# Performance work log

Measured on AMD Instinct MI355X. Metric: run time of the kernel, lower is better.

Reference implementation:

```python
import jax, jax.numpy as jnp
import numpy as np

DIM = 1024
NUM_HEADS = 16
HEAD_DIM = DIM // NUM_HEADS
SCALE = HEAD_DIM ** -0.5


def setup_inputs() -> dict:
    key = jax.random.key(0)
    ks = jax.random.split(key, 5)
    x = jax.random.normal(ks[0], (4, 1024, DIM), dtype=jnp.float32)
    w_qkv = jax.random.normal(ks[1], (DIM, 3 * DIM), dtype=jnp.float32) * (DIM ** -0.5)
    b_qkv = jnp.zeros((3 * DIM,), dtype=jnp.float32)
    w_proj = jax.random.normal(ks[2], (DIM, DIM), dtype=jnp.float32) * (DIM ** -0.5)
    b_proj = jnp.zeros((DIM,), dtype=jnp.float32)
    return {"x": x, "w_qkv": w_qkv, "b_qkv": b_qkv, "w_proj": w_proj, "b_proj": b_proj}


def reference(x, w_qkv, b_qkv, w_proj, b_proj):
    B, N, C = x.shape
    qkv = x @ w_qkv + b_qkv                                  # [B, N, 3C]
    qkv = qkv.reshape(B, N, 3, NUM_HEADS, HEAD_DIM)
    qkv = jnp.transpose(qkv, (2, 0, 3, 1, 4))                # [3, B, H, N, d]
    q, k, v = qkv[0] * SCALE, qkv[1], qkv[2]
    # attn scores in float32 (clamp to finfo range is a no-op after the cast)
    attn = jnp.einsum('bhnd,bhmd->bhnm', q, k).astype(jnp.float32)
    f32 = jnp.finfo(jnp.float32)
    attn = jnp.clip(attn, f32.min, f32.max)
    attn = jax.nn.softmax(attn, axis=-1)
    out = jnp.einsum('bhnm,bhmd->bhnd', attn, v)             # [B, H, N, d]
    out = jnp.transpose(out, (0, 2, 1, 3)).reshape(B, N, C)
    return out @ w_proj + b_proj
```

## Files before the change

### kernel.cpp

```cpp
#include <hip/hip_runtime.h>


typedef _Float16 half8 __attribute__((ext_vector_type(8)));
typedef _Float16 half4v __attribute__((ext_vector_type(4)));
typedef float floatx4 __attribute__((ext_vector_type(4)));

#define MFMA16(a, b, c) __builtin_amdgcn_mfma_f32_16x16x32_f16((a), (b), (c), 0, 0, 0)

static constexpr int DIM = 1024;
static constexpr int BATCH = 4;
static constexpr int SEQ = 1024;
static constexpr int NH = 16;
static constexpr int HD = 64;
static constexpr float SCALE = 0.125f;

__device__ static inline void gld16(_Float16* lds, const _Float16* g) {
    __builtin_amdgcn_global_load_lds(
        (const __attribute__((address_space(1))) void*)g,
        (__attribute__((address_space(3))) void*)lds, 16, 0, 0);
}

__global__ __launch_bounds__(256) void prep(const float* __restrict__ x,
                                            _Float16* __restrict__ xh,
                                            const float* __restrict__ wqkv,
                                            _Float16* __restrict__ wqkvT,
                                            const float* __restrict__ wproj,
                                            _Float16* __restrict__ wprojT) {
    __shared__ float tile[32][33];
    const int bid = blockIdx.x;
    const int tid = threadIdx.x;
    if (bid < 4096) {
        int i = (bid * 256 + tid) * 4;
        float4 v = *reinterpret_cast<const float4*>(x + i);
        half4v h;
        h[0] = (_Float16)v.x; h[1] = (_Float16)v.y;
        h[2] = (_Float16)v.z; h[3] = (_Float16)v.w;
        const int m = i >> 10, k = i & 1023;
        *reinterpret_cast<half4v*>(
            &xh[((size_t)(k >> 5) * 4096 + m) * 32 + (k & 31)]) = h;
        return;
    }
    const float* in;
    _Float16* out;
    int C, NN, bx, by;
    if (bid < 7168) {
        int b = bid - 4096;
        in = wqkv; out = wqkvT; C = 3072; NN = 3072;
        bx = b % 96; by = b / 96;
    } else {
        int b = bid - 7168;
        in = wproj; out = wprojT; C = 1024; NN = 1024;
        bx = b & 31; by = b >> 5;
    }
    const int c0 = bx * 32, r0 = by * 32;
    const int tx = tid & 31, ty = tid >> 5;
#pragma unroll
    for (int j = 0; j < 32; j += 8)
        tile[ty + j][tx] = in[(size_t)(r0 + ty + j) * C + (c0 + tx)];
    __syncthreads();
#pragma unroll
    for (int j = 0; j < 32; j += 8)
        out[((size_t)(r0 >> 5) * NN + (c0 + ty + j)) * 32 + tx] =
            (_Float16)tile[tx][ty + j];
}

template <int MODE>
__global__ __launch_bounds__(256, 2) void gemm_bt(const _Float16* __restrict__ A,
                                                  const _Float16* __restrict__ Bt,
                                                  const float* __restrict__ bias, int N,
                                                  float* __restrict__ outF,
                                                  _Float16* __restrict__ qbuf,
                                                  _Float16* __restrict__ kbuf,
                                                  _Float16* __restrict__ vtbuf) {
    constexpr int NT = 32;
    __shared__ _Float16 Ah[3 * 4096];
    __shared__ _Float16 Bh[3 * 4096];

    const int tid = threadIdx.x;
    const int wid = tid >> 6;
    const int lane = tid & 63;
    const int g = lane >> 4;
    const int ln = lane & 15;
    const int wr = wid >> 1, wc = wid & 1;
    const int m0 = blockIdx.y * 128;
    const int n0 = blockIdx.x * 128;
    const size_t PA = (size_t)4096 * 32;
    const size_t PB = (size_t)N * 32;
    const int woff = wid * 1024;
    const int lsw = (lane >> 2) * 32 + (((lane & 3) ^ ((lane >> 3) & 3)) * 8);
    const int gsw = (g ^ ((ln >> 1) & 3)) * 8;
    const _Float16* ga = A + (size_t)m0 * 32 + woff + lsw;
    const _Float16* gb = Bt + (size_t)n0 * 32 + woff + lsw;

    floatx4 acc[4][4];
#pragma unroll
    for (int i = 0; i < 4; ++i)
#pragma unroll
        for (int j = 0; j < 4; ++j) acc[i][j] = (floatx4){0.f, 0.f, 0.f, 0.f};

#pragma unroll
    for (int t = 0; t < 2; ++t) {
        gld16(&Ah[t * 4096 + woff], ga + t * PA);
        gld16(&Ah[t * 4096 + woff + 512], ga + t * PA + 512);
        gld16(&Bh[t * 4096 + woff], gb + t * PB);
        gld16(&Bh[t * 4096 + woff + 512], gb + t * PB + 512);
    }

    for (int kt = 0; kt < NT; ++kt) {
        if (kt < NT - 1) asm volatile("s_waitcnt vmcnt(4)" ::: "memory");
        else             asm volatile("s_waitcnt vmcnt(0)" ::: "memory");
        asm volatile("s_barrier" ::: "memory");
        if (kt < NT - 2) {
            const int pf = (kt + 2) % 3;
            const size_t ka = (size_t)(kt + 2) * PA;
            const size_t kb = (size_t)(kt + 2) * PB;
            gld16(&Ah[pf * 4096 + woff], ga + ka);
            gld16(&Ah[pf * 4096 + woff + 512], ga + ka + 512);
            gld16(&Bh[pf * 4096 + woff], gb + kb);
            gld16(&Bh[pf * 4096 + woff + 512], gb + kb + 512);
        }
        const _Float16* Ac = &Ah[(kt % 3) * 4096];
        const _Float16* Bc = &Bh[(kt % 3) * 4096];

        half8 af[4], bf[4];
#pragma unroll
        for (int i = 0; i < 4; ++i)
            af[i] = *reinterpret_cast<const half8*>(
                &Ac[(wr * 64 + i * 16 + ln) * 32 + gsw]);
#pragma unroll
        for (int j = 0; j < 4; ++j)
            bf[j] = *reinterpret_cast<const half8*>(
                &Bc[(wc * 64 + j * 16 + ln) * 32 + gsw]);
#pragma unroll
        for (int i = 0; i < 4; ++i)
#pragma unroll
            for (int j = 0; j < 4; ++j) acc[i][j] = MFMA16(af[i], bf[j], acc[i][j]);
    }

#pragma unroll
    for (int i = 0; i < 4; ++i) {
#pragma unroll
        for (int j = 0; j < 4; ++j) {
            const int n = n0 + wc * 64 + j * 16 + ln;
            const float bn = bias[n];
            const int mrow = m0 + wr * 64 + i * 16 + g * 4;
            if (MODE == 0) {
                const int which = n >> 10;
                const int rem = n & 1023;
                const int h = rem >> 6;
                const int dd = rem & 63;
                const int b = mrow >> 10, tok = mrow & 1023;
                const int bh = b * NH + h;
                if (which == 2) {
                    half4v pk;
#pragma unroll
                    for (int r = 0; r < 4; ++r) pk[r] = (_Float16)(acc[i][j][r] + bn);
                    *reinterpret_cast<half4v*>(
                        &vtbuf[((size_t)(bh * 32 + (tok >> 5)) * 64 + dd) * 32 +
                               (tok & 31)]) = pk;
                } else if (which == 1) {
#pragma unroll
                    for (int r = 0; r < 4; ++r)
                        kbuf[((size_t)(bh * 2 + (dd >> 5)) * SEQ + tok + r) * 32 +
                             (dd & 31)] = (_Float16)(acc[i][j][r] + bn);
                } else {
#pragma unroll
                    for (int r = 0; r < 4; ++r)
                        qbuf[(size_t)((bh << 10) + tok + r) * HD + dd] =
                            (_Float16)((acc[i][j][r] + bn) * SCALE);
                }
            } else {
#pragma unroll
                for (int r = 0; r < 4; ++r)
                    outF[(size_t)(mrow + r) * N + n] = acc[i][j][r] + bn;
            }
        }
    }
}

__global__ __launch_bounds__(256, 2) void flash_attn(const _Float16* __restrict__ qbuf,
                                                     const _Float16* __restrict__ kbuf,
                                                     const _Float16* __restrict__ vtbuf,
                                                     _Float16* __restrict__ attn_out) {
    __shared__ _Float16 Klds[3 * 4096];
    __shared__ _Float16 Vlds[3 * 4096];
    __shared__ _Float16 Plds[8 * 16 * 68];

    const int tid = threadIdx.x;
    const int wid = tid >> 6;
    const int lane = tid & 63;
    const int g = lane >> 4;
    const int ln = lane & 15;
    const int bh = blockIdx.x;
    const int qbase = blockIdx.y * 128 + wid * 32;
    const _Float16* qg = qbuf + ((size_t)bh << 10) * HD;
    const _Float16* kg = kbuf + (size_t)bh * (2 * SEQ * 32);
    const _Float16* vg = vtbuf + (size_t)bh * (32 * 64 * 32);

    const int woff = wid * 512;
    const int lsw = (lane >> 2) * 32 + (((lane & 3) ^ ((lane >> 3) & 3)) * 8);
    const int gsw = (g ^ ((ln >> 1) & 3)) * 8;

    half8 qf[2][2];
#pragma unroll
    for (int rg = 0; rg < 2; ++rg)
#pragma unroll
        for (int f = 0; f < 2; ++f)
            qf[rg][f] = *reinterpret_cast<const half8*>(
                qg + (size_t)(qbase + rg * 16 + ln) * HD + f * 32 + g * 8);

    floatx4 o[2][4];
#pragma unroll
    for (int rg = 0; rg < 2; ++rg)
#pragma unroll
        for (int t = 0; t < 4; ++t) o[rg][t] = (floatx4){0.f, 0.f, 0.f, 0.f};
    float l_lane[2][4] = {{0.f, 0.f, 0.f, 0.f}, {0.f, 0.f, 0.f, 0.f}};

    _Float16* Pw = Plds + wid * (2 * 16 * 68);

    constexpr int NT = SEQ / 64;
#pragma unroll
    for (int t = 0; t < 2; ++t) {
#pragma unroll
        for (int f = 0; f < 2; ++f) {
            gld16(&Klds[t * 4096 + f * 2048 + woff],
                  kg + (size_t)f * (SEQ * 32) + t * 64 * 32 + woff + lsw);
            gld16(&Vlds[t * 4096 + f * 2048 + woff],
                  vg + (size_t)(2 * t + f) * 2048 + woff + lsw);
        }
    }

    for (int kt = 0; kt < NT; ++kt) {
        if (kt < NT - 1) asm volatile("s_waitcnt vmcnt(4)" ::: "memory");
        else             asm volatile("s_waitcnt vmcnt(0)" ::: "memory");
        asm volatile("s_barrier" ::: "memory");
        if (kt < NT - 2) {
            const int pf = (kt + 2) % 3;
            const int krp = (kt + 2) * 64;
#pragma unroll
            for (int f = 0; f < 2; ++f) {
                gld16(&Klds[pf * 4096 + f * 2048 + woff],
                      kg + (size_t)f * (SEQ * 32) + krp * 32 + woff + lsw);
                gld16(&Vlds[pf * 4096 + f * 2048 + woff],
                      vg + (size_t)(2 * (kt + 2) + f) * 2048 + woff + lsw);
            }
        }
        const _Float16* Kb = &Klds[(kt % 3) * 4096];
        const _Float16* Vb = &Vlds[(kt % 3) * 4096];

        half8 kf[4][2], vf[4][2];
#pragma unroll
        for (int c = 0; c < 4; ++c)
#pragma unroll
            for (int f = 0; f < 2; ++f) {
                kf[c][f] = *reinterpret_cast<const half8*>(
                    &Kb[f * 2048 + (c * 16 + ln) * 32 + gsw]);
                vf[c][f] = *reinterpret_cast<const half8*>(
                    &Vb[f * 2048 + (c * 16 + ln) * 32 + gsw]);
            }

        floatx4 s[2][4];
#pragma unroll
        for (int rg = 0; rg < 2; ++rg)
#pragma unroll
            for (int c = 0; c < 4; ++c) {
                floatx4 z = (floatx4){0.f, 0.f, 0.f, 0.f};
                z = MFMA16(qf[rg][0], kf[c][0], z);
                z = MFMA16(qf[rg][1], kf[c][1], z);
                s[rg][c] = z;
            }

#pragma unroll
        for (int rg = 0; rg < 2; ++rg)
#pragma unroll
            for (int c = 0; c < 4; ++c)
#pragma unroll
                for (int r = 0; r < 4; ++r) {
                    float p = __expf(s[rg][c][r]);
                    l_lane[rg][r] += p;
                    Pw[(rg * 16 + g * 4 + r) * 68 + c * 16 + ln] = (_Float16)p;
                }

        asm volatile("s_waitcnt lgkmcnt(0)" ::: "memory");

#pragma unroll
        for (int rg = 0; rg < 2; ++rg) {
            half8 pf0 = *reinterpret_cast<const half8*>(&Pw[(rg * 16 + ln) * 68 + g * 8]);
            half8 pf1 = *reinterpret_cast<const half8*>(&Pw[(rg * 16 + ln) * 68 + 32 + g * 8]);
#pragma unroll
            for (int t = 0; t < 4; ++t) {
                o[rg][t] = MFMA16(pf0, vf[t][0], o[rg][t]);
                o[rg][t] = MFMA16(pf1, vf[t][1], o[rg][t]);
            }
        }
    }

    const int b = bh >> 4, h = bh & 15;
#pragma unroll
    for (int rg = 0; rg < 2; ++rg)
#pragma unroll
        for (int r = 0; r < 4; ++r) {
            float l = l_lane[rg][r];
            l += __shfl_xor(l, 1);
            l += __shfl_xor(l, 2);
            l += __shfl_xor(l, 4);
            l += __shfl_xor(l, 8);
            const float inv = 1.0f / l;
            const int tok = qbase + rg * 16 + g * 4 + r;
#pragma unroll
            for (int t = 0; t < 4; ++t)
                attn_out[((size_t)(h * 2 + (t >> 1)) * 4096 + (b * SEQ + tok)) * 32 +
                         (t & 1) * 16 + ln] = (_Float16)(o[rg][t][r] * inv);
        }
}

extern "C" void kernel_launch(void* const* d_in, const int* in_sizes, int n_in,
                              void* d_out, int out_size, void* d_ws, size_t ws_size,
                              hipStream_t stream) {
    const float* x = (const float*)d_in[0];
    const float* wqkv = (const float*)d_in[1];
    const float* bqkv = (const float*)d_in[2];
    const float* wproj = (const float*)d_in[3];
    const float* bproj = (const float*)d_in[4];
    float* out = (float*)d_out;

    char* ws = (char*)d_ws;
    _Float16* xh     = (_Float16*)(ws);
    _Float16* wqkvT  = (_Float16*)(ws + (8ull << 20));
    _Float16* qbuf   = (_Float16*)(ws + (14ull << 20));
    _Float16* kbuf   = (_Float16*)(ws + (22ull << 20));
    _Float16* vtbuf  = (_Float16*)(ws + (30ull << 20));
    _Float16* wprojT = (_Float16*)(ws + (38ull << 20));
    _Float16* attn   = xh;

    prep<<<8192, 256, 0, stream>>>(x, xh, wqkv, wqkvT, wproj, wprojT);
    gemm_bt<0><<<dim3(24, 32), 256, 0, stream>>>(xh, wqkvT, bqkv, 3 * DIM, nullptr,
                                                 qbuf, kbuf, vtbuf);
    flash_attn<<<dim3(BATCH * NH, SEQ / 128), 256, 0, stream>>>(qbuf, kbuf, vtbuf, attn);
    gemm_bt<1><<<dim3(8, 32), 256, 0, stream>>>(attn, wprojT, bproj, DIM, out,
                                                nullptr, nullptr, nullptr);
}
```

Baseline: 181.6 us.

## Compute transposed scores and pass P through lane shuffles instead of LDS

Flash attention now computes S^T = K·Q^T so each wave handles 16 query rows. The fp16-packed probabilities are rearranged into the A-operand layout with cross-lane shuffles, which removes the per-wave P scratch in LDS and its write/read round trip. The K/V pipeline drops from triple to double buffering with a full vmcnt(0) wait each iteration. The grid doubles with launch bounds raised to 4 blocks per CU. This trades less K/V reuse per block and a shallower prefetch for lower LDS use, fewer registers and more occupancy.

Result: faster. 177.2 us (-2.4%).

```diff
diff --git a/kernel.cpp b/kernel.cpp
--- a/kernel.cpp
+++ b/kernel.cpp
@@ -3,6 +3,7 @@
 
 typedef _Float16 half8 __attribute__((ext_vector_type(8)));
 typedef _Float16 half4v __attribute__((ext_vector_type(4)));
+typedef __fp16 fp16x2 __attribute__((ext_vector_type(2)));
 typedef float floatx4 __attribute__((ext_vector_type(4)));
 
 #define MFMA16(a, b, c) __builtin_amdgcn_mfma_f32_16x16x32_f16((a), (b), (c), 0, 0, 0)
@@ -178,13 +179,12 @@
     }
 }
 
-__global__ __launch_bounds__(256, 2) void flash_attn(const _Float16* __restrict__ qbuf,
+__global__ __launch_bounds__(256, 4) void flash_attn(const _Float16* __restrict__ qbuf,
                                                      const _Float16* __restrict__ kbuf,
                                                      const _Float16* __restrict__ vtbuf,
                                                      _Float16* __restrict__ attn_out) {
-    __shared__ _Float16 Klds[3 * 4096];
-    __shared__ _Float16 Vlds[3 * 4096];
-    __shared__ _Float16 Plds[8 * 16 * 68];
+    __shared__ _Float16 Klds[2 * 4096];
+    __shared__ _Float16 Vlds[2 * 4096];
 
     const int tid = threadIdx.x;
     const int wid = tid >> 6;
@@ -192,7 +192,7 @@
     const int g = lane >> 4;
     const int ln = lane & 15;
     const int bh = blockIdx.x;
-    const int qbase = blockIdx.y * 128 + wid * 32;
+    const int qbase = blockIdx.y * 64 + wid * 16;
     const _Float16* qg = qbuf + ((size_t)bh << 10) * HD;
     const _Float16* kg = kbuf + (size_t)bh * (2 * SEQ * 32);
     const _Float16* vg = vtbuf + (size_t)bh * (32 * 64 * 32);
@@ -200,53 +200,43 @@
     const int woff = wid * 512;
     const int lsw = (lane >> 2) * 32 + (((lane & 3) ^ ((lane >> 3) & 3)) * 8);
     const int gsw = (g ^ ((ln >> 1) & 3)) * 8;
-
-    half8 qf[2][2];
-#pragma unroll
-    for (int rg = 0; rg < 2; ++rg)
-#pragma unroll
-        for (int f = 0; f < 2; ++f)
-            qf[rg][f] = *reinterpret_cast<const half8*>(
-                qg + (size_t)(qbase + rg * 16 + ln) * HD + f * 32 + g * 8);
-
-    floatx4 o[2][4];
-#pragma unroll
-    for (int rg = 0; rg < 2; ++rg)
-#pragma unroll
-        for (int t = 0; t < 4; ++t) o[rg][t] = (floatx4){0.f, 0.f, 0.f, 0.f};
-    float l_lane[2][4] = {{0.f, 0.f, 0.f, 0.f}, {0.f, 0.f, 0.f, 0.f}};
-
-    _Float16* Pw = Plds + wid * (2 * 16 * 68);
+    const int sl0 = ((lane >> 4) & 1) * 32 + ln;
+    const bool hi32 = (lane & 32) != 0;
+
+    half8 qf[2];
+#pragma unroll
+    for (int f = 0; f < 2; ++f)
+        qf[f] = *reinterpret_cast<const half8*>(
+            qg + (size_t)(qbase + ln) * HD + f * 32 + g * 8);
+
+    floatx4 o[4];
+#pragma unroll
+    for (int t = 0; t < 4; ++t) o[t] = (floatx4){0.f, 0.f, 0.f, 0.f};
+    float l_lane = 0.f;
 
     constexpr int NT = SEQ / 64;
 #pragma unroll
-    for (int t = 0; t < 2; ++t) {
-#pragma unroll
-        for (int f = 0; f < 2; ++f) {
-            gld16(&Klds[t * 4096 + f * 2048 + woff],
-                  kg + (size_t)f * (SEQ * 32) + t * 64 * 32 + woff + lsw);
-            gld16(&Vlds[t * 4096 + f * 2048 + woff],
-                  vg + (size_t)(2 * t + f) * 2048 + woff + lsw);
-        }
+    for (int f = 0; f < 2; ++f) {
+        gld16(&Klds[f * 2048 + woff], kg + (size_t)f * (SEQ * 32) + woff + lsw);
+        gld16(&Vlds[f * 2048 + woff], vg + (size_t)f * 2048 + woff + lsw);
     }
 
     for (int kt = 0; kt < NT; ++kt) {
-        if (kt < NT - 1) asm volatile("s_waitcnt vmcnt(4)" ::: "memory");
-        else             asm volatile("s_waitcnt vmcnt(0)" ::: "memory");
+        asm volatile("s_waitcnt vmcnt(0)" ::: "memory");
         asm volatile("s_barrier" ::: "memory");
-        if (kt < NT - 2) {
-            const int pf = (kt + 2) % 3;
-            const int krp = (kt + 2) * 64;
+        const int cur = kt & 1;
+        if (kt < NT - 1) {
+            const int nb = cur ^ 1;
 #pragma unroll
             for (int f = 0; f < 2; ++f) {
-                gld16(&Klds[pf * 4096 + f * 2048 + woff],
-                      kg + (size_t)f * (SEQ * 32) + krp * 32 + woff + lsw);
-                gld16(&Vlds[pf * 4096 + f * 2048 + woff],
-                      vg + (size_t)(2 * (kt + 2) + f) * 2048 + woff + lsw);
+                gld16(&Klds[nb * 4096 + f * 2048 + woff],
+                      kg + (size_t)f * (SEQ * 32) + (kt + 1) * 2048 + woff + lsw);
+                gld16(&Vlds[nb * 4096 + f * 2048 + woff],
+                      vg + (size_t)(2 * (kt + 1) + f) * 2048 + woff + lsw);
             }
         }
-        const _Float16* Kb = &Klds[(kt % 3) * 4096];
-        const _Float16* Vb = &Vlds[(kt % 3) * 4096];
+        const _Float16* Kb = &Klds[cur * 4096];
+        const _Float16* Vb = &Vlds[cur * 4096];
 
         half8 kf[4][2], vf[4][2];
 #pragma unroll
@@ -259,59 +249,59 @@
                     &Vb[f * 2048 + (c * 16 + ln) * 32 + gsw]);
             }
 
-        floatx4 s[2][4];
-#pragma unroll
-        for (int rg = 0; rg < 2; ++rg)
-#pragma unroll
-            for (int c = 0; c < 4; ++c) {
-                floatx4 z = (floatx4){0.f, 0.f, 0.f, 0.f};
-                z = MFMA16(qf[rg][0], kf[c][0], z);
-                z = MFMA16(qf[rg][1], kf[c][1], z);
-                s[rg][c] = z;
-            }
-
-#pragma unroll
-        for (int rg = 0; rg < 2; ++rg)
-#pragma unroll
-            for (int c = 0; c < 4; ++c)
-#pragma unroll
-                for (int r = 0; r < 4; ++r) {
-                    float p = __expf(s[rg][c][r]);
-                    l_lane[rg][r] += p;
-                    Pw[(rg * 16 + g * 4 + r) * 68 + c * 16 + ln] = (_Float16)p;
-                }
-
-        asm volatile("s_waitcnt lgkmcnt(0)" ::: "memory");
-
-#pragma unroll
-        for (int rg = 0; rg < 2; ++rg) {
-            half8 pf0 = *reinterpret_cast<const half8*>(&Pw[(rg * 16 + ln) * 68 + g * 8]);
-            half8 pf1 = *reinterpret_cast<const half8*>(&Pw[(rg * 16 + ln) * 68 + 32 + g * 8]);
-#pragma unroll
-            for (int t = 0; t < 4; ++t) {
-                o[rg][t] = MFMA16(pf0, vf[t][0], o[rg][t]);
-                o[rg][t] = MFMA16(pf1, vf[t][1], o[rg][t]);
-            }
-        }
-    }
+        floatx4 st[4];
+#pragma unroll
+        for (int c = 0; c < 4; ++c) {
+            floatx4 z = (floatx4){0.f, 0.f, 0.f, 0.f};
+            z = MFMA16(kf[c][0], qf[0], z);
+            z = MFMA16(kf[c][1], qf[1], z);
+            st[c] = z;
+        }
+
+        int pk[4][2];
+#pragma unroll
+        for (int c = 0; c < 4; ++c) {
+            float p0 = __expf(st[c][0]);
+            float p1 = __expf(st[c][1]);
+            float p2 = __expf(st[c][2]);
+            float p3 = __expf(st[c][3]);
+            l_lane += (p0 + p1) + (p2 + p3);
+            union { fp16x2 h; int i; } u0, u1;
+            u0.h = __builtin_amdgcn_cvt_pkrtz(p0, p1);
+            u1.h = __builtin_amdgcn_cvt_pkrtz(p2, p3);
+            pk[c][0] = u0.i;
+            pk[c][1] = u1.i;
+        }
+
+#pragma unroll
+        for (int H = 0; H < 2; ++H) {
+            int a0 = __shfl(pk[2 * H][0], sl0), b0 = __shfl(pk[2 * H + 1][0], sl0);
+            int a1 = __shfl(pk[2 * H][1], sl0), b1 = __shfl(pk[2 * H + 1][1], sl0);
+            int a2 = __shfl(pk[2 * H][0], sl0 + 16), b2 = __shfl(pk[2 * H + 1][0], sl0 + 16);
+            int a3 = __shfl(pk[2 * H][1], sl0 + 16), b3 = __shfl(pk[2 * H + 1][1], sl0 + 16);
+            union { int i[4]; half8 h; } ua;
+            ua.i[0] = hi32 ? b0 : a0;
+            ua.i[1] = hi32 ? b1 : a1;
+            ua.i[2] = hi32 ? b2 : a2;
+            ua.i[3] = hi32 ? b3 : a3;
+#pragma unroll
+            for (int t = 0; t < 4; ++t) o[t] = MFMA16(ua.h, vf[t][H], o[t]);
+        }
+    }
+
+    l_lane += __shfl_xor(l_lane, 16);
+    l_lane += __shfl_xor(l_lane, 32);
 
     const int b = bh >> 4, h = bh & 15;
 #pragma unroll
-    for (int rg = 0; rg < 2; ++rg)
-#pragma unroll
-        for (int r = 0; r < 4; ++r) {
-            float l = l_lane[rg][r];
-            l += __shfl_xor(l, 1);
-            l += __shfl_xor(l, 2);
-            l += __shfl_xor(l, 4);
-            l += __shfl_xor(l, 8);
-            const float inv = 1.0f / l;
-            const int tok = qbase + rg * 16 + g * 4 + r;
-#pragma unroll
-            for (int t = 0; t < 4; ++t)
-                attn_out[((size_t)(h * 2 + (t >> 1)) * 4096 + (b * SEQ + tok)) * 32 +
-                         (t & 1) * 16 + ln] = (_Float16)(o[rg][t][r] * inv);
-        }
+    for (int r = 0; r < 4; ++r) {
+        const float inv = 1.0f / __shfl(l_lane, g * 4 + r);
+        const int tok = qbase + g * 4 + r;
+#pragma unroll
+        for (int t = 0; t < 4; ++t)
+            attn_out[((size_t)(h * 2 + (t >> 1)) * 4096 + (b * SEQ + tok)) * 32 +
+                     (t & 1) * 16 + ln] = (_Float16)(o[t][r] * inv);
+    }
 }
 
 extern "C" void kernel_launch(void* const* d_in, const int* in_sizes, int n_in,
@@ -336,7 +326,7 @@
     prep<<<8192, 256, 0, stream>>>(x, xh, wqkv, wqkvT, wproj, wprojT);
     gemm_bt<0><<<dim3(24, 32), 256, 0, stream>>>(xh, wqkvT, bqkv, 3 * DIM, nullptr,
                                                  qbuf, kbuf, vtbuf);
-    flash_attn<<<dim3(BATCH * NH, SEQ / 128), 256, 0, stream>>>(qbuf, kbuf, vtbuf, attn);
+    flash_attn<<<dim3(BATCH * NH, SEQ / 64), 256, 0, stream>>>(qbuf, kbuf, vtbuf, attn);
     gemm_bt<1><<<dim3(8, 32), 256, 0, stream>>>(attn, wprojT, bproj, DIM, out,
                                                 nullptr, nullptr, nullptr);
 }
```
